# Kernel optimization log

Measured on AMD Instinct MI355X. Metric: run time of the kernel, lower is better.

The kernel has to match this reference:

```python
import jax, jax.numpy as jnp
import numpy as np

N = 100000
E = 1600000
F_IN = 256
F_OUT = 128
ALPHA = 0.2  # leaky relu slope


def setup_inputs() -> dict:
    key = jax.random.key(0)
    ks = jax.random.split(key, 8)
    x = jax.random.normal(ks[0], (N, F_IN), dtype=jnp.float32)
    edge_index = jax.random.randint(ks[1], (2, E), 0, N, dtype=jnp.int64)
    edge_attr = jax.random.normal(ks[2], (E,), dtype=jnp.float32)
    # xavier-normal-ish params
    weight = jax.random.normal(ks[3], (F_IN, F_OUT), dtype=jnp.float32) * (1.414 * np.sqrt(2.0 / (F_IN + F_OUT)))
    bias = jnp.zeros((F_OUT,), dtype=jnp.float32)
    a_l = jax.random.normal(ks[4], (F_OUT,), dtype=jnp.float32) * 0.1
    a_r = jax.random.normal(ks[5], (F_OUT,), dtype=jnp.float32) * 0.1
    fc = jax.random.normal(ks[6], (F_OUT, 1), dtype=jnp.float32) * (1.414 * np.sqrt(2.0 / (F_OUT + 1)))
    bf = jnp.zeros((1,), dtype=jnp.float32)
    return {"x": x, "edge_index": edge_index, "edge_attr": edge_attr,
            "weight": weight, "bias": bias, "a_l": a_l, "a_r": a_r,
            "fc": fc, "bf": bf}


def _segment_softmax(val, seg, num_segments):
    # numerically stable softmax over edges grouped by destination row
    seg_max = jax.ops.segment_max(val, seg, num_segments=num_segments)
    val = jnp.exp(val - seg_max[seg])
    seg_sum = jax.ops.segment_sum(val, seg, num_segments=num_segments)
    return val / (seg_sum[seg] + 1e-16)


def reference(x, edge_index, edge_attr, weight, bias, a_l, a_r, fc, bf):
    # dropout layers are identity in eval mode (deterministic reference)
    h = x @ weight                                   # [N, F_OUT]
    row, col = edge_index[0], edge_index[1]          # dst, src
    # GAT-style edge attention: leaky_relu(a_l.h[dst] + a_r.h[src])
    score_l = h @ a_l                                # [N]
    score_r = h @ a_r                                # [N]
    e = score_l[row] + score_r[col]                  # [E]
    e = jnp.where(e > 0, e, ALPHA * e)
    # row-softmax normalization over incoming edges of each dst node
    val = _segment_softmax(e, row, N)                # [E]
    # spmm: out[i] = sum_{(i,j) in E} val_ij * h[j]
    val_h = jax.ops.segment_sum(val[:, None] * h[col], row, num_segments=N)  # [N, F_OUT]
    val_h = jnp.where(jnp.isnan(val_h), 0.0, val_h)
    val_h = val_h + bias
    # NodeAdaptiveEncoder: relu(x) + sigmoid(x@fc + bf) * min(x, 0)
    gate = jax.nn.sigmoid(val_h @ fc + bf)           # [N, 1]
    out = jnp.where(val_h < 0, 0.0, val_h) + gate * jnp.where(val_h > 0, 0.0, val_h)
    return out
```

## Files before the change

### kernel.cpp

```cpp
#include <hip/hip_runtime.h>

#define N_NODES 100000
#define N_EDGES 1600000
#define FIN 256
#define FOUT 128
#define LRELU_ALPHA 0.2f

#define NBUCKET 391
#define PBLOCKS 256
#define PCHUNK  (N_EDGES / PBLOCKS)
#define BCAP    5120

using bf16x8 = __attribute__((ext_vector_type(8))) short;
using f32x4  = __attribute__((ext_vector_type(4))) float;
using v2f    = __attribute__((ext_vector_type(2))) float;

static __device__ __forceinline__ unsigned short f2bf(float f) {
    union { float f; unsigned u; } v; v.f = f;
    unsigned r = (v.u + 0x7FFF + ((v.u >> 16) & 1)) >> 16;
    return (unsigned short)r;
}

static __device__ __forceinline__ bf16x8 cvt8(float4 a, float4 b) {
    union { bf16x8 v; unsigned short u[8]; } r;
    r.u[0] = f2bf(a.x); r.u[1] = f2bf(a.y); r.u[2] = f2bf(a.z); r.u[3] = f2bf(a.w);
    r.u[4] = f2bf(b.x); r.u[5] = f2bf(b.y); r.u[6] = f2bf(b.z); r.u[7] = f2bf(b.w);
    return r.v;
}

static __device__ __forceinline__ void gld_lds16(const unsigned short* g, unsigned short* l) {
    __builtin_amdgcn_global_load_lds(
        (const __attribute__((address_space(1))) unsigned int*)g,
        (__attribute__((address_space(3))) unsigned int*)l, 16, 0, 0);
}

static __device__ __forceinline__ v2f up2(unsigned u) {
    v2f r;
    r.x = __int_as_float((int)(u << 16));
    r.y = __int_as_float((int)(u & 0xFFFF0000u));
    return r;
}

__global__ void k_wt(const float* __restrict__ w, unsigned short* __restrict__ wt_sw,
                     int* __restrict__ bcnt)
{
    if (blockIdx.x == 0)
        for (int z = threadIdx.x; z < NBUCKET; z += 256) bcnt[z] = 0;
    int i = blockIdx.x * blockDim.x + threadIdx.x;
    if (i >= FIN * FOUT) return;
    int k = i >> 7, n = i & 127;
    wt_sw[n * FIN + (((k >> 3) ^ (n & 7)) << 3) + (k & 7)] = f2bf(w[k * FOUT + n]);
}

__global__ __launch_bounds__(256, 2) void k_gemm3(
    const float* __restrict__ x, const unsigned short* __restrict__ wt_sw,
    const float* __restrict__ a_l, const float* __restrict__ a_r,
    unsigned short* __restrict__ hb, float* __restrict__ score_l,
    float* __restrict__ score_r)
{
    __shared__ unsigned short wlds[FOUT * FIN];

    const int tid  = threadIdx.x;
    const int lane = tid & 63;
    const int wid  = tid >> 6;
    const int m    = lane & 15;
    const int q    = lane >> 4;

    {
        const unsigned short* g = wt_sw + wid * 8192;
        unsigned short*       l = wlds  + wid * 8192;
#pragma unroll
        for (int i = 0; i < 16; ++i)
            gld_lds16(g + i * 512 + lane * 8, l + i * 512);
    }

    const int row0 = blockIdx.x * 128 + wid * 32;
    int r0 = row0 + m;       if (r0 > N_NODES - 1) r0 = N_NODES - 1;
    int r1 = row0 + 16 + m;  if (r1 > N_NODES - 1) r1 = N_NODES - 1;
    const float* xp0 = x + (long)r0 * FIN + q * 8;
    const float* xp1 = x + (long)r1 * FIN + q * 8;

    float4 xb[2][2][2];
    xb[0][0][0] = *(const float4*)(xp0);        xb[0][0][1] = *(const float4*)(xp0 + 4);
    xb[0][1][0] = *(const float4*)(xp1);        xb[0][1][1] = *(const float4*)(xp1 + 4);
    xb[1][0][0] = *(const float4*)(xp0 + 32);   xb[1][0][1] = *(const float4*)(xp0 + 36);
    xb[1][1][0] = *(const float4*)(xp1 + 32);   xb[1][1][1] = *(const float4*)(xp1 + 36);

    f32x4 acc[2][8];
#pragma unroll
    for (int mt = 0; mt < 2; ++mt)
#pragma unroll
        for (int nt = 0; nt < 8; ++nt) acc[mt][nt] = (f32x4){0.f, 0.f, 0.f, 0.f};

    __syncthreads();

    const int xr = m & 7;

    bf16x8 bfr[2][8];
#pragma unroll
    for (int nt = 0; nt < 8; ++nt)
        bfr[0][nt] = *(const bf16x8*)&wlds[(nt * 16 + m) * FIN + ((q ^ xr) << 3)];

#pragma unroll
    for (int s = 0; s < 8; ++s) {
        const int p = s & 1;
        bf16x8 a0 = cvt8(xb[p][0][0], xb[p][0][1]);
        bf16x8 a1 = cvt8(xb[p][1][0], xb[p][1][1]);
        if (s + 2 < 8) {
            xb[p][0][0] = *(const float4*)(xp0 + (s + 2) * 32);
            xb[p][0][1] = *(const float4*)(xp0 + (s + 2) * 32 + 4);
            xb[p][1][0] = *(const float4*)(xp1 + (s + 2) * 32);
            xb[p][1][1] = *(const float4*)(xp1 + (s + 2) * 32 + 4);
        }
        if (s + 1 < 8) {
#pragma unroll
            for (int nt = 0; nt < 8; ++nt)
                bfr[1 - p][nt] = *(const bf16x8*)
                    &wlds[(nt * 16 + m) * FIN + ((((s + 1) * 4 + q) ^ xr) << 3)];
        }
#pragma unroll
        for (int nt = 0; nt < 8; ++nt) {
            acc[0][nt] = __builtin_amdgcn_mfma_f32_16x16x32_bf16(a0, bfr[p][nt], acc[0][nt], 0, 0, 0);
            acc[1][nt] = __builtin_amdgcn_mfma_f32_16x16x32_bf16(a1, bfr[p][nt], acc[1][nt], 0, 0, 0);
        }
    }

    float al[8], ar[8];
#pragma unroll
    for (int nt = 0; nt < 8; ++nt) { al[nt] = a_l[nt * 16 + m]; ar[nt] = a_r[nt * 16 + m]; }

#pragma unroll
    for (int mt = 0; mt < 2; ++mt) {
#pragma unroll
        for (int r = 0; r < 4; ++r) {
            const int node = row0 + mt * 16 + q * 4 + r;
            const bool ok = node < N_NODES;
            float sl = 0.f, sr = 0.f;
#pragma unroll
            for (int nt = 0; nt < 8; ++nt) {
                float v = acc[mt][nt][r];
                if (ok) hb[node * FOUT + nt * 16 + m] = f2bf(v);
                sl = fmaf(v, al[nt], sl);
                sr = fmaf(v, ar[nt], sr);
            }
#pragma unroll
            for (int msk = 1; msk < 16; msk <<= 1) {
                sl += __shfl_xor(sl, msk, 64);
                sr += __shfl_xor(sr, msk, 64);
            }
            if (ok && m == 0) { score_l[node] = sl; score_r[node] = sr; }
        }
    }
}

__global__ __launch_bounds__(512) void k_part(const int* __restrict__ ei,
                                              int* __restrict__ bcnt,
                                              unsigned* __restrict__ part)
{
    __shared__ unsigned staging[PCHUNK];
    __shared__ unsigned short bkt[PCHUNK];
    __shared__ int cnt[512];
    __shared__ int loc[512];
    __shared__ int gbase[NBUCKET];

    const int tid = threadIdx.x;
    const int e0  = blockIdx.x * PCHUNK;

    cnt[tid] = 0;
    __syncthreads();

    for (int i = tid; i < PCHUNK; i += 512)
        atomicAdd(&cnt[ei[e0 + i] >> 8], 1);
    __syncthreads();

    int v = cnt[tid];
    loc[tid] = v;
    __syncthreads();
    for (int off = 1; off < 512; off <<= 1) {
        int t = (tid >= off) ? loc[tid - off] : 0;
        __syncthreads();
        loc[tid] += t;
        __syncthreads();
    }
    int excl = loc[tid] - v;
    if (tid < NBUCKET && v > 0) gbase[tid] = atomicAdd(&bcnt[tid], v);
    loc[tid] = excl;
    cnt[tid] = excl;
    __syncthreads();

    for (int i = tid; i < PCHUNK; i += 512) {
        int dst = ei[e0 + i];
        int src = ei[N_EDGES + e0 + i];
        int b = dst >> 8;
        unsigned rec = ((unsigned)(dst & 255) << 17) | (unsigned)src;
        int p = atomicAdd(&cnt[b], 1);
        staging[p] = rec;
        bkt[p] = (unsigned short)b;
    }
    __syncthreads();

    for (int i = tid; i < PCHUNK; i += 512) {
        int b = bkt[i];
        int off = gbase[b] + (i - loc[b]);
        if (off < BCAP) part[b * BCAP + off] = staging[i];
    }
}

__global__ __launch_bounds__(512) void k_bucket(const unsigned* __restrict__ part,
                                                const int* __restrict__ bcnt,
                                                int* __restrict__ rowbeg,
                                                int* __restrict__ rowend,
                                                unsigned* __restrict__ csrs)
{
    __shared__ unsigned rin[BCAP];
    __shared__ unsigned rs[BCAP];
    __shared__ int hist[256];
    __shared__ int tmp[512];

    const int b   = blockIdx.x;
    const int tid = threadIdx.x;
    const int beg = b * BCAP;
    int cnt = bcnt[b];
    if (cnt > BCAP) cnt = BCAP;
    const int d0 = b << 8;

    if (tid < 256) hist[tid] = 0;
    __syncthreads();

    for (int i = tid; i < cnt; i += 512) {
        unsigned rec = part[beg + i];
        rin[i] = rec;
        atomicAdd(&hist[rec >> 17], 1);
    }
    __syncthreads();

    int v = (tid < 256) ? hist[tid] : 0;
    tmp[tid] = v;
    __syncthreads();
    for (int off = 1; off < 512; off <<= 1) {
        int t = (tid >= off) ? tmp[tid - off] : 0;
        __syncthreads();
        tmp[tid] += t;
        __syncthreads();
    }
    if (tid < 256) {
        int excl = tmp[tid] - v;
        hist[tid] = excl;
        int d = d0 + tid;
        if (d < N_NODES) { rowbeg[d] = beg + excl; rowend[d] = beg + excl + v; }
    }
    __syncthreads();

    for (int i = tid; i < cnt; i += 512) {
        unsigned rec = rin[i];
        int p = atomicAdd(&hist[rec >> 17], 1);
        rs[p] = rec;
    }
    __syncthreads();

    for (int i = tid; i < cnt; i += 512)
        csrs[beg + i] = rs[i];
}

__global__ __launch_bounds__(256) void k_spmm_gate(
    const int* __restrict__ rowbeg, const int* __restrict__ rowend,
    const unsigned* __restrict__ csrs,
    const unsigned short* __restrict__ hb,
    const float* __restrict__ score_l, const float* __restrict__ score_r,
    const float* __restrict__ bias, const float* __restrict__ fc,
    const float* __restrict__ bf, float* __restrict__ out)
{
    const int t    = threadIdx.x & 15;
    const int node = blockIdx.x * 16 + (threadIdx.x >> 4);
    if (node >= N_NODES) return;

    const int beg = rowbeg[node], end = rowend[node];
    const float sl = score_l[node];

    v2f acc0 = {0.f, 0.f}, acc1 = {0.f, 0.f}, acc2 = {0.f, 0.f}, acc3 = {0.f, 0.f};
    float denom = 0.f;

    for (int j = beg; j < end; j += 2) {
        bool h2 = (j + 1) < end;
        unsigned r0 = csrs[j];
        unsigned r1 = h2 ? csrs[j + 1] : r0;
        int s0 = r0 & 0x1FFFF;
        int s1 = r1 & 0x1FFFF;
        float e0 = sl + score_r[s0];
        float e1 = sl + score_r[s1];
        e0 = e0 > 0.f ? e0 : LRELU_ALPHA * e0;
        e1 = e1 > 0.f ? e1 : LRELU_ALPHA * e1;
        float w0 = __expf(e0);
        float w1 = h2 ? __expf(e1) : 0.f;
        uint4 g0 = *(const uint4*)&hb[s0 * FOUT + t * 8];
        uint4 g1 = *(const uint4*)&hb[s1 * FOUT + t * 8];
        denom += w0 + w1;
        v2f w02 = {w0, w0}, w12 = {w1, w1};
        acc0 += w02 * up2(g0.x);  acc1 += w02 * up2(g0.y);
        acc2 += w02 * up2(g0.z);  acc3 += w02 * up2(g0.w);
        acc0 += w12 * up2(g1.x);  acc1 += w12 * up2(g1.y);
        acc2 += w12 * up2(g1.z);  acc3 += w12 * up2(g1.w);
    }

    float inv = 1.0f / (denom + 1e-16f);

    float vx[8];
    vx[0] = acc0.x; vx[1] = acc0.y; vx[2] = acc1.x; vx[3] = acc1.y;
    vx[4] = acc2.x; vx[5] = acc2.y; vx[6] = acc3.x; vx[7] = acc3.y;

    float gp = 0.f;
#pragma unroll
    for (int i = 0; i < 8; ++i) {
        vx[i] = fmaf(vx[i], inv, bias[t * 8 + i]);
        gp = fmaf(vx[i], fc[t * 8 + i], gp);
    }
#pragma unroll
    for (int msk = 1; msk < 16; msk <<= 1) gp += __shfl_xor(gp, msk, 64);
    float g = 1.0f / (1.0f + __expf(-(gp + bf[0])));

    float4 o0, o1;
    float* ov0 = &o0.x; float* ov1 = &o1.x;
#pragma unroll
    for (int i = 0; i < 4; ++i) {
        float v2 = vx[i];
        ov0[i] = (v2 < 0.f ? 0.f : v2) + g * (v2 > 0.f ? 0.f : v2);
    }
#pragma unroll
    for (int i = 0; i < 4; ++i) {
        float v2 = vx[4 + i];
        ov1[i] = (v2 < 0.f ? 0.f : v2) + g * (v2 > 0.f ? 0.f : v2);
    }
    *(float4*)&out[node * FOUT + t * 8]     = o0;
    *(float4*)&out[node * FOUT + t * 8 + 4] = o1;
}

extern "C" void kernel_launch(void* const* d_in, const int* in_sizes, int n_in,
                              void* d_out, int out_size, void* d_ws, size_t ws_size,
                              hipStream_t stream)
{
    const float* x      = (const float*)d_in[0];
    const int*   ei     = (const int*)d_in[1];
    const float* weight = (const float*)d_in[3];
    const float* bias   = (const float*)d_in[4];
    const float* a_l    = (const float*)d_in[5];
    const float* a_r    = (const float*)d_in[6];
    const float* fc     = (const float*)d_in[7];
    const float* bf     = (const float*)d_in[8];
    float* out = (float*)d_out;

    char* ws = (char*)d_ws;
    unsigned short* hb      = (unsigned short*)(ws);
    unsigned short* wt_sw   = (unsigned short*)(ws + 25600000);
    float*          score_l = (float*)(ws + 25665536);
    float*          score_r = (float*)(ws + 26065536);
    int*            bcnt    = (int*)  (ws + 26465536);
    int*            rowbeg  = (int*)  (ws + 26467584);
    int*            rowend  = (int*)  (ws + 26867584);
    unsigned*       part    = (unsigned*)(ws + 27267584);
    unsigned*       csrs    = (unsigned*)(ws + 35275264);

    k_wt<<<(FIN * FOUT + 255) / 256, 256, 0, stream>>>(weight, wt_sw, bcnt);

    k_gemm3<<<(N_NODES + 127) / 128, 256, 0, stream>>>(
        x, wt_sw, a_l, a_r, hb, score_l, score_r);

    k_part<<<PBLOCKS, 512, 0, stream>>>(ei, bcnt, part);
    k_bucket<<<NBUCKET, 512, 0, stream>>>(part, bcnt, rowbeg, rowend, csrs);

    k_spmm_gate<<<(N_NODES + 15) / 16, 256, 0, stream>>>(
        rowbeg, rowend, csrs, hb, score_l, score_r, bias, fc, bf, out);
}
```

Measured before the change: 295.9 us.

## Split each node's edges across four 16-lane groups with software-pipelined gathers

The SpMM/gate kernel now assigns a full 64-lane wavefront per destination node instead of 16 lanes. Four lane groups each handle every fourth edge, and the next record, score and row are prefetched one iteration ahead. Partial sums are then combined with cross-group shuffles, and groups 0 and 1 each write half of the output. The goal is more memory-level parallelism and less latency per node on the random row gathers. The cost is four times as many wavefronts, extra shuffle reductions, and idle lanes for low-degree nodes (average degree is 16).

```diff
diff --git a/kernel.cpp b/kernel.cpp
--- a/kernel.cpp
+++ b/kernel.cpp
@@ -270,68 +270,104 @@
     const float* __restrict__ bias, const float* __restrict__ fc,
     const float* __restrict__ bf, float* __restrict__ out)
 {
-    const int t    = threadIdx.x & 15;
-    const int node = blockIdx.x * 16 + (threadIdx.x >> 4);
+    const int lane = threadIdx.x & 63;
+    const int g    = lane >> 4;
+    const int t    = lane & 15;
+    const int node = blockIdx.x * 4 + (threadIdx.x >> 6);
     if (node >= N_NODES) return;
 
     const int beg = rowbeg[node], end = rowend[node];
+    const int deg = end - beg;
     const float sl = score_l[node];
 
-    v2f acc0 = {0.f, 0.f}, acc1 = {0.f, 0.f}, acc2 = {0.f, 0.f}, acc3 = {0.f, 0.f};
+    v2f a0 = {0.f, 0.f}, a1 = {0.f, 0.f}, a2 = {0.f, 0.f}, a3 = {0.f, 0.f};
     float denom = 0.f;
 
-    for (int j = beg; j < end; j += 2) {
-        bool h2 = (j + 1) < end;
-        unsigned r0 = csrs[j];
-        unsigned r1 = h2 ? csrs[j + 1] : r0;
-        int s0 = r0 & 0x1FFFF;
-        int s1 = r1 & 0x1FFFF;
-        float e0 = sl + score_r[s0];
-        float e1 = sl + score_r[s1];
-        e0 = e0 > 0.f ? e0 : LRELU_ALPHA * e0;
-        e1 = e1 > 0.f ? e1 : LRELU_ALPHA * e1;
-        float w0 = __expf(e0);
-        float w1 = h2 ? __expf(e1) : 0.f;
-        uint4 g0 = *(const uint4*)&hb[s0 * FOUT + t * 8];
-        uint4 g1 = *(const uint4*)&hb[s1 * FOUT + t * 8];
-        denom += w0 + w1;
-        v2f w02 = {w0, w0}, w12 = {w1, w1};
-        acc0 += w02 * up2(g0.x);  acc1 += w02 * up2(g0.y);
-        acc2 += w02 * up2(g0.z);  acc3 += w02 * up2(g0.w);
-        acc0 += w12 * up2(g1.x);  acc1 += w12 * up2(g1.y);
-        acc2 += w12 * up2(g1.z);  acc3 += w12 * up2(g1.w);
-    }
-
-    float inv = 1.0f / (denom + 1e-16f);
+    if (deg > 0) {
+        const int nit  = (deg + 3) >> 2;
+        const int last = end - 1;
+
+        int j = beg + g;
+        int jc = j <= last ? j : last;
+        unsigned recA = csrs[jc];
+        unsigned recB = recA;
+        if (nit > 1) {
+            int j1 = j + 4;
+            int jc1 = j1 <= last ? j1 : last;
+            recB = csrs[jc1];
+        }
+        int   sA   = recA & 0x1FFFF;
+        float srA  = score_r[sA];
+        uint4 rowA = *(const uint4*)&hb[sA * FOUT + t * 8];
+        bool  vA   = j < end;
+
+        for (int i = 0; i < nit; ++i) {
+            unsigned recC = recB;
+            if (i + 2 < nit) {
+                int j2 = j + 8;
+                int jc2 = j2 <= last ? j2 : last;
+                recC = csrs[jc2];
+            }
+            float srB = 0.f;
+            uint4 rowB = {0u, 0u, 0u, 0u};
+            bool  vB = false;
+            if (i + 1 < nit) {
+                int sB = recB & 0x1FFFF;
+                srB  = score_r[sB];
+                rowB = *(const uint4*)&hb[sB * FOUT + t * 8];
+                vB   = (j + 4) < end;
+            }
+            float e = sl + srA;
+            e = e > 0.f ? e : LRELU_ALPHA * e;
+            float w = vA ? __expf(e) : 0.f;
+            denom += w;
+            v2f w2 = {w, w};
+            a0 += w2 * up2(rowA.x);  a1 += w2 * up2(rowA.y);
+            a2 += w2 * up2(rowA.z);  a3 += w2 * up2(rowA.w);
+            recB = recC; srA = srB; rowA = rowB; vA = vB;
+            j += 4;
+        }
+    }
+
+    float accf[8] = {a0.x, a0.y, a1.x, a1.y, a2.x, a2.y, a3.x, a3.y};
+#pragma unroll
+    for (int k = 0; k < 8; ++k) {
+        accf[k] += __shfl_xor(accf[k], 16, 64);
+        accf[k] += __shfl_xor(accf[k], 32, 64);
+    }
+    denom += __shfl_xor(denom, 16, 64);
+    denom += __shfl_xor(denom, 32, 64);
+
+    const float inv = 1.0f / (denom + 1e-16f);
 
     float vx[8];
-    vx[0] = acc0.x; vx[1] = acc0.y; vx[2] = acc1.x; vx[3] = acc1.y;
-    vx[4] = acc2.x; vx[5] = acc2.y; vx[6] = acc3.x; vx[7] = acc3.y;
-
     float gp = 0.f;
 #pragma unroll
     for (int i = 0; i < 8; ++i) {
-        vx[i] = fmaf(vx[i], inv, bias[t * 8 + i]);
+        vx[i] = fmaf(accf[i], inv, bias[t * 8 + i]);
         gp = fmaf(vx[i], fc[t * 8 + i], gp);
     }
 #pragma unroll
     for (int msk = 1; msk < 16; msk <<= 1) gp += __shfl_xor(gp, msk, 64);
-    float g = 1.0f / (1.0f + __expf(-(gp + bf[0])));
-
-    float4 o0, o1;
-    float* ov0 = &o0.x; float* ov1 = &o1.x;
-#pragma unroll
-    for (int i = 0; i < 4; ++i) {
-        float v2 = vx[i];
-        ov0[i] = (v2 < 0.f ? 0.f : v2) + g * (v2 > 0.f ? 0.f : v2);
-    }
-#pragma unroll
-    for (int i = 0; i < 4; ++i) {
-        float v2 = vx[4 + i];
-        ov1[i] = (v2 < 0.f ? 0.f : v2) + g * (v2 > 0.f ? 0.f : v2);
-    }
-    *(float4*)&out[node * FOUT + t * 8]     = o0;
-    *(float4*)&out[node * FOUT + t * 8 + 4] = o1;
+    const float gate = 1.0f / (1.0f + __expf(-(gp + bf[0])));
+
+    float4 o;
+    float* ov = &o.x;
+    if (g == 0) {
+#pragma unroll
+        for (int i = 0; i < 4; ++i) {
+            float v2 = vx[i];
+            ov[i] = (v2 < 0.f ? 0.f : v2) + gate * (v2 > 0.f ? 0.f : v2);
+        }
+        *(float4*)&out[node * FOUT + t * 8] = o;
+    } else if (g == 1) {
+#pragma unroll
+        for (int i = 0; i < 4; ++i) {
+            float v2 = vx[4 + i];
+            ov[i] = (v2 < 0.f ? 0.f : v2) + gate * (v2 > 0.f ? 0.f : v2);
+        }
+        *(float4*)&out[node * FOUT + t * 8 + 4] = o;
+    }
 }
 
 extern "C" void kernel_launch(void* const* d_in, const int* in_sizes, int n_in,
@@ -367,6 +403,6 @@
     k_part<<<PBLOCKS, 512, 0, stream>>>(ei, bcnt, part);
     k_bucket<<<NBUCKET, 512, 0, stream>>>(part, bcnt, rowbeg, rowend, csrs);
 
-    k_spmm_gate<<<(N_NODES + 15) / 16, 256, 0, stream>>>(
+    k_spmm_gate<<<(N_NODES + 3) / 4, 256, 0, stream>>>(
         rowbeg, rowend, csrs, hb, score_l, score_r, bias, fc, bf, out);
 }
```

Result: no change. 294.8 us (-0.4%).

## Rewrite SpMM aggregation as per-16-node MFMA with segment-max stable softmax

Applied to the files above, without the earlier changes.

Replaces the per-node scalar gather-accumulate SpMM with a kernel that gives each 64-thread block 16 consecutive destination nodes. It builds a 16x32 bf16 weight tile and a 32x128 gathered-feature tile in LDS per 32-edge chunk and reduces them with MFMA bf16 instructions, computing the softmax denominator with an MFMA against ones. Per-node max subtraction is added via an atomicMax pass, and the scores are pre-scaled by log2e so the kernel can call exp2f. The costs are an extra pass over the edges, block-level syncs, bf16 rounding of the attention weights, and one block per 16 nodes with the launch assuming N is divisible by 16.

```diff
diff --git a/kernel.cpp b/kernel.cpp
--- a/kernel.cpp
+++ b/kernel.cpp
@@ -5,6 +5,7 @@
 #define FIN 256
 #define FOUT 128
 #define LRELU_ALPHA 0.2f
+#define LOG2E 1.4426950408889634f
 
 #define NBUCKET 391
 #define PBLOCKS 256
@@ -13,7 +14,6 @@
 
 using bf16x8 = __attribute__((ext_vector_type(8))) short;
 using f32x4  = __attribute__((ext_vector_type(4))) float;
-using v2f    = __attribute__((ext_vector_type(2))) float;
 
 static __device__ __forceinline__ unsigned short f2bf(float f) {
     union { float f; unsigned u; } v; v.f = f;
@@ -32,13 +32,6 @@
     __builtin_amdgcn_global_load_lds(
         (const __attribute__((address_space(1))) unsigned int*)g,
         (__attribute__((address_space(3))) unsigned int*)l, 16, 0, 0);
-}
-
-static __device__ __forceinline__ v2f up2(unsigned u) {
-    v2f r;
-    r.x = __int_as_float((int)(u << 16));
-    r.y = __int_as_float((int)(u & 0xFFFF0000u));
-    return r;
 }
 
 __global__ void k_wt(const float* __restrict__ w, unsigned short* __restrict__ wt_sw,
@@ -148,7 +141,10 @@
                 sl += __shfl_xor(sl, msk, 64);
                 sr += __shfl_xor(sr, msk, 64);
             }
-            if (ok && m == 0) { score_l[node] = sl; score_r[node] = sr; }
+            if (ok && m == 0) {
+                score_l[node] = sl * LOG2E;
+                score_r[node] = sr * LOG2E;
+            }
         }
     }
 }
@@ -262,7 +258,7 @@
         csrs[beg + i] = rs[i];
 }
 
-__global__ __launch_bounds__(256) void k_spmm_gate(
+__global__ __launch_bounds__(64, 4) void k_spmm_mfma(
     const int* __restrict__ rowbeg, const int* __restrict__ rowend,
     const unsigned* __restrict__ csrs,
     const unsigned short* __restrict__ hb,
@@ -270,68 +266,133 @@
     const float* __restrict__ bias, const float* __restrict__ fc,
     const float* __restrict__ bf, float* __restrict__ out)
 {
-    const int t    = threadIdx.x & 15;
-    const int node = blockIdx.x * 16 + (threadIdx.x >> 4);
-    if (node >= N_NODES) return;
-
-    const int beg = rowbeg[node], end = rowend[node];
-    const float sl = score_l[node];
-
-    v2f acc0 = {0.f, 0.f}, acc1 = {0.f, 0.f}, acc2 = {0.f, 0.f}, acc3 = {0.f, 0.f};
-    float denom = 0.f;
-
-    for (int j = beg; j < end; j += 2) {
-        bool h2 = (j + 1) < end;
-        unsigned r0 = csrs[j];
-        unsigned r1 = h2 ? csrs[j + 1] : r0;
-        int s0 = r0 & 0x1FFFF;
-        int s1 = r1 & 0x1FFFF;
-        float e0 = sl + score_r[s0];
-        float e1 = sl + score_r[s1];
-        e0 = e0 > 0.f ? e0 : LRELU_ALPHA * e0;
-        e1 = e1 > 0.f ? e1 : LRELU_ALPHA * e1;
-        float w0 = __expf(e0);
-        float w1 = h2 ? __expf(e1) : 0.f;
-        uint4 g0 = *(const uint4*)&hb[s0 * FOUT + t * 8];
-        uint4 g1 = *(const uint4*)&hb[s1 * FOUT + t * 8];
-        denom += w0 + w1;
-        v2f w02 = {w0, w0}, w12 = {w1, w1};
-        acc0 += w02 * up2(g0.x);  acc1 += w02 * up2(g0.y);
-        acc2 += w02 * up2(g0.z);  acc3 += w02 * up2(g0.w);
-        acc0 += w12 * up2(g1.x);  acc1 += w12 * up2(g1.y);
-        acc2 += w12 * up2(g1.z);  acc3 += w12 * up2(g1.w);
-    }
-
-    float inv = 1.0f / (denom + 1e-16f);
-
-    float vx[8];
-    vx[0] = acc0.x; vx[1] = acc0.y; vx[2] = acc1.x; vx[3] = acc1.y;
-    vx[4] = acc2.x; vx[5] = acc2.y; vx[6] = acc3.x; vx[7] = acc3.y;
-
-    float gp = 0.f;
-#pragma unroll
-    for (int i = 0; i < 8; ++i) {
-        vx[i] = fmaf(vx[i], inv, bias[t * 8 + i]);
-        gp = fmaf(vx[i], fc[t * 8 + i], gp);
-    }
-#pragma unroll
-    for (int msk = 1; msk < 16; msk <<= 1) gp += __shfl_xor(gp, msk, 64);
-    float g = 1.0f / (1.0f + __expf(-(gp + bf[0])));
-
-    float4 o0, o1;
-    float* ov0 = &o0.x; float* ov1 = &o1.x;
-#pragma unroll
-    for (int i = 0; i < 4; ++i) {
-        float v2 = vx[i];
-        ov0[i] = (v2 < 0.f ? 0.f : v2) + g * (v2 > 0.f ? 0.f : v2);
-    }
-#pragma unroll
-    for (int i = 0; i < 4; ++i) {
-        float v2 = vx[4 + i];
-        ov1[i] = (v2 < 0.f ? 0.f : v2) + g * (v2 > 0.f ? 0.f : v2);
-    }
-    *(float4*)&out[node * FOUT + t * 8]     = o0;
-    *(float4*)&out[node * FOUT + t * 8 + 4] = o1;
+    __shared__ __align__(16) unsigned short Alds[16 * 40];
+    __shared__ __align__(16) char Blds[8 * 1296];
+    __shared__ unsigned MxI[16];
+    __shared__ float    MxSr[16];
+
+    const int lane = threadIdx.x;
+    const int t    = lane & 15;
+    const int q    = lane >> 4;
+    const int kk   = lane & 31;
+    const int d0   = blockIdx.x << 4;
+
+    const int beg = rowbeg[d0];
+    const int end = rowend[d0 + 15];
+    const int L   = end - beg;
+
+    f32x4 acc[8], den;
+#pragma unroll
+    for (int nb = 0; nb < 8; ++nb) acc[nb] = (f32x4){0.f, 0.f, 0.f, 0.f};
+    den = (f32x4){0.f, 0.f, 0.f, 0.f};
+
+    const bf16x8 onesb = {(short)0x3F80, (short)0x3F80, (short)0x3F80, (short)0x3F80,
+                          (short)0x3F80, (short)0x3F80, (short)0x3F80, (short)0x3F80};
+
+    if (L > 0) {
+        const int T    = (L + 31) >> 5;
+        const int last = end - 1;
+
+        if (lane < 16) MxI[lane] = 0u;
+        __syncthreads();
+        for (int tt = 0; tt < T; ++tt) {
+            int idx = beg + (tt << 5) + kk; if (idx > last) idx = last;
+            unsigned rec = csrs[idx];
+            if (lane < 32) {
+                unsigned u = __float_as_uint(score_r[rec & 0x1FFFF]);
+                unsigned key = u ^ ((unsigned)((int)u >> 31) | 0x80000000u);
+                atomicMax(&MxI[(rec >> 17) & 15], key);
+            }
+        }
+        __syncthreads();
+        if (lane < 16) {
+            unsigned kx = MxI[lane];
+            MxSr[lane] = __uint_as_float((kx & 0x80000000u) ? (kx ^ 0x80000000u) : ~kx);
+        }
+        __syncthreads();
+
+        const unsigned selperm = (t & 1) ? 0x07060302u : 0x05040100u;
+
+        for (int tt = 0; tt < T; ++tt) {
+            const int e0 = tt << 5;
+            int idx = beg + e0 + kk; if (idx > last) idx = last;
+            unsigned rec = csrs[idx];
+            int src = rec & 0x1FFFF;
+            int m   = (rec >> 17) & 15;
+
+            float sl = score_l[d0 + m];
+            float e  = sl + score_r[src];
+            float lv = fmaxf(e, LRELU_ALPHA * e);
+            float em = sl + MxSr[m];
+            float rm = fmaxf(em, LRELU_ALPHA * em);
+            float w  = (kk < L - e0) ? exp2f(lv - rm) : 0.f;
+            unsigned short wh = f2bf(w);
+
+            uint4 gv[8];
+#pragma unroll
+            for (int i = 0; i < 8; ++i) {
+                int ix = beg + e0 + i * 4 + q; if (ix > last) ix = last;
+                int s2 = csrs[ix] & 0x1FFFF;
+                gv[i] = *(const uint4*)((const char*)hb + (s2 << 8) + (t << 4));
+            }
+
+            __syncthreads();
+            *(uint4*)((char*)Alds + lane * 16) = make_uint4(0u, 0u, 0u, 0u);
+            if (lane < 16)
+                *(uint4*)((char*)Alds + 1024 + lane * 16) = make_uint4(0u, 0u, 0u, 0u);
+            if (lane < 32) Alds[m * 40 + kk] = wh;
+            {
+                char* bw = Blds + (t >> 1) * 1296 + ((t & 1) << 4) + q * 40;
+#pragma unroll
+                for (int i = 0; i < 8; ++i) {
+                    *(uint2*)(bw + i * 160)     = make_uint2(gv[i].x, gv[i].y);
+                    *(uint2*)(bw + i * 160 + 8) = make_uint2(gv[i].z, gv[i].w);
+                }
+            }
+            __syncthreads();
+
+            bf16x8 af = *(const bf16x8*)&Alds[t * 40 + q * 8];
+            den = __builtin_amdgcn_mfma_f32_16x16x32_bf16(af, onesb, den, 0, 0, 0);
+
+            const char* br = Blds + ((t & ~1) << 1) + q * 320;
+#pragma unroll
+            for (int nb = 0; nb < 8; ++nb) {
+                union { unsigned u[4]; bf16x8 v; } bu;
+#pragma unroll
+                for (int p = 0; p < 4; ++p) {
+                    unsigned lo = *(const unsigned*)(br + nb * 1296 + (2 * p) * 40);
+                    unsigned hi = *(const unsigned*)(br + nb * 1296 + (2 * p + 1) * 40);
+                    bu.u[p] = __builtin_amdgcn_perm(hi, lo, selperm);
+                }
+                acc[nb] = __builtin_amdgcn_mfma_f32_16x16x32_bf16(af, bu.v, acc[nb], 0, 0, 0);
+            }
+        }
+    }
+
+    float bfv = bf[0];
+    float bia[8], fcv[8];
+#pragma unroll
+    for (int nb = 0; nb < 8; ++nb) { bia[nb] = bias[nb * 16 + t]; fcv[nb] = fc[nb * 16 + t]; }
+#pragma unroll
+    for (int r = 0; r < 4; ++r) {
+        float inv = 1.0f / (den[r] + 1e-16f);
+        float vx[8], gp = 0.f;
+#pragma unroll
+        for (int nb = 0; nb < 8; ++nb) {
+            vx[nb] = fmaf(acc[nb][r], inv, bia[nb]);
+            gp = fmaf(vx[nb], fcv[nb], gp);
+        }
+#pragma unroll
+        for (int msk = 1; msk < 16; msk <<= 1) gp += __shfl_xor(gp, msk, 64);
+        float gate = 1.0f / (1.0f + __expf(-(gp + bfv)));
+        const int row = d0 + q * 4 + r;
+#pragma unroll
+        for (int nb = 0; nb < 8; ++nb) {
+            float v = vx[nb];
+            out[row * FOUT + nb * 16 + t] =
+                (v < 0.f ? 0.f : v) + gate * (v > 0.f ? 0.f : v);
+        }
+    }
 }
 
 extern "C" void kernel_launch(void* const* d_in, const int* in_sizes, int n_in,
@@ -367,6 +428,6 @@
     k_part<<<PBLOCKS, 512, 0, stream>>>(ei, bcnt, part);
     k_bucket<<<NBUCKET, 512, 0, stream>>>(part, bcnt, rowbeg, rowend, csrs);
 
-    k_spmm_gate<<<(N_NODES + 15) / 16, 256, 0, stream>>>(
+    k_spmm_mfma<<<N_NODES / 16, 64, 0, stream>>>(
         rowbeg, rowend, csrs, hb, score_l, score_r, bias, fc, bf, out);
 }
```

Measured after the change: 301.4 us. About the same (+1.8%).
